# Optimization experiments

Measured on AMD Instinct MI355X. Metric: run time of the kernel, lower is better.

The kernel has to match this reference:

```python
import jax, jax.numpy as jnp
import numpy as np

N_NODES = 50000
N_EDGES = 800000
N_GRAPHS = 1024
H = 128          # hidden_dim
L = 5            # n_conv_layers
NODE_IN = 4
EDGE_IN = 41
N_TARGETS = 3
EPS = 1e-5


def _ln(x, g, b):
    m = jnp.mean(x, axis=-1, keepdims=True)
    v = jnp.var(x, axis=-1, keepdims=True)
    return (x - m) / jnp.sqrt(v + EPS) * g + b


def setup_inputs() -> dict:
    key = jax.random.key(0)
    ks = jax.random.split(key, 24)
    w = lambda k, shp: (jax.random.normal(k, shp, dtype=jnp.float32) * 0.05)
    inp = {
        "atom_fea": jax.random.normal(ks[0], (N_NODES, NODE_IN), dtype=jnp.float32),
        "nbr_fea": jax.random.normal(ks[1], (N_EDGES, EDGE_IN), dtype=jnp.float32),
        "nbr_idx": jax.random.randint(ks[2], (N_EDGES, 2), 0, N_NODES, dtype=jnp.int32),
        "batch_mapping": jnp.sort(jax.random.randint(ks[3], (N_NODES,), 0, N_GRAPHS, dtype=jnp.int32)),
        # node embedding: Linear(4->H) + LayerNorm + SiLU
        "emb_w": w(ks[4], (NODE_IN, H)), "emb_b": jnp.zeros((H,), jnp.float32),
        "emb_ln_g": jnp.ones((H,), jnp.float32), "emb_ln_b": jnp.zeros((H,), jnp.float32),
        # edge embedding: Linear(41->H) + SiLU
        "edge_w": w(ks[5], (EDGE_IN, H)), "edge_b": jnp.zeros((H,), jnp.float32),
        # conv layers: Linear(2H->2H), SiLU, Linear(2H->H), SiLU; stacked over L
        "conv_w1": w(ks[6], (L, 2 * H, 2 * H)), "conv_b1": jnp.zeros((L, 2 * H), jnp.float32),
        "conv_w2": w(ks[7], (L, 2 * H, H)), "conv_b2": jnp.zeros((L, H), jnp.float32),
        "ln_g": jnp.ones((L, H), jnp.float32), "ln_b": jnp.zeros((L, H), jnp.float32),
        # output head
        "out_w1": w(ks[8], (H, H)), "out_b1": jnp.zeros((H,), jnp.float32),
        "out_w2": w(ks[9], (H, H // 2)), "out_b2": jnp.zeros((H // 2,), jnp.float32),
        "out_w3": w(ks[10], (H // 2, N_TARGETS)), "out_b3": jnp.zeros((N_TARGETS,), jnp.float32),
    }
    return inp


def reference(atom_fea, nbr_fea, nbr_idx, batch_mapping,
              emb_w, emb_b, emb_ln_g, emb_ln_b, edge_w, edge_b,
              conv_w1, conv_b1, conv_w2, conv_b2, ln_g, ln_b,
              out_w1, out_b1, out_w2, out_b2, out_w3, out_b3):
    silu = jax.nn.silu
    # embeddings (dropout is eval-mode identity)
    x = silu(_ln(atom_fea @ emb_w + emb_b, emb_ln_g, emb_ln_b))      # [N, H]
    e = silu(nbr_fea @ edge_w + edge_b)                               # [E, H]
    src, dst = nbr_idx[:, 0], nbr_idx[:, 1]
    n = x.shape[0]
    # per-node incoming edge counts (same every layer)
    cnt = jax.ops.segment_sum(jnp.ones_like(dst, dtype=x.dtype), dst, num_segments=n)
    cnt = jnp.clip(cnt, 1.0)[:, None]
    for i in range(L):
        m = jnp.concatenate([x[src], e], axis=1)                      # [E, 2H] gather
        m = silu(m @ conv_w1[i] + conv_b1[i])                         # [E, 2H]
        m = silu(m @ conv_w2[i] + conv_b2[i])                         # [E, H]
        aggr = jax.ops.segment_sum(m, dst, num_segments=n) / cnt      # scatter-mean
        x = _ln(x + aggr, ln_g[i], ln_b[i])                           # residual + LN
    # graph-level mean pooling
    gcnt = jax.ops.segment_sum(jnp.ones((n,), x.dtype), batch_mapping, num_segments=N_GRAPHS)
    gcnt = jnp.clip(gcnt, 1.0)[:, None]
    crystal = jax.ops.segment_sum(x, batch_mapping, num_segments=N_GRAPHS) / gcnt  # [G, H]
    h = silu(crystal @ out_w1 + out_b1)
    h = silu(h @ out_w2 + out_b2)
    return h @ out_w3 + out_b3                                        # [G, n_targets]
```

## Files before the change

### kernel.cpp

```cpp
#include <hip/hip_runtime.h>
#include <hip/hip_bf16.h>
#include <math.h>

#define N_NODES 50000
#define N_EDGES 800000
#define N_GRAPHS 1024
#define HD 128
#define NLAYERS 5
#define EDGE_IN 41
#define NT 3
#define LN_EPS 1e-5f

typedef unsigned int uint;
typedef unsigned short ushort;
typedef __attribute__((ext_vector_type(8))) short short8;
typedef __attribute__((ext_vector_type(4))) float f32x4;
typedef __attribute__((ext_vector_type(4))) ushort us4;

__device__ __forceinline__ float silu_f(float v) {
    return v * __builtin_amdgcn_rcpf(1.0f + __expf(-v));
}

__device__ __forceinline__ ushort f2bf(float f) {
    uint u = __float_as_uint(f);
    u = u + 0x7FFFu + ((u >> 16) & 1u);
    return (ushort)(u >> 16);
}

__device__ __forceinline__ short8 ld16(const ushort* p) {
    union { int4 i; short8 s; } u;
    u.i = *(const int4*)p;
    return u.s;
}

__device__ __forceinline__ f32x4 mfma16(short8 a, short8 b, f32x4 c) {
    return __builtin_amdgcn_mfma_f32_16x16x32_bf16(a, b, c, 0, 0, 0);
}

__device__ __forceinline__ void compiler_fence() {
    __asm__ volatile("" ::: "memory");
}

__device__ __forceinline__ void cp16(const ushort* g, ushort* l) {
    __builtin_amdgcn_global_load_lds(
        (const __attribute__((address_space(1))) unsigned int*)g,
        (__attribute__((address_space(3))) unsigned int*)l, 16, 0, 0);
}

__device__ __forceinline__ void stage4k(ushort* lds, const ushort* g, int w, int L) {
#pragma unroll
    for (int i = 0; i < 2; ++i) {
        int f = w * 1024 + i * 512;
        cp16(g + f + L * 8, lds + f);
    }
}

__global__ void k_zero(float* __restrict__ p, int n) {
    int i = blockIdx.x * 256 + threadIdx.x;
    if (i < n) p[i] = 0.0f;
}

__global__ void k_hist(const int* __restrict__ nbr_idx, int* __restrict__ cnt_i) {
    int i = blockIdx.x * 256 + threadIdx.x;
    if (i < N_EDGES) atomicAdd(&cnt_i[nbr_idx[2 * i + 1]], 1);
}

__global__ __launch_bounds__(1024) void k_scan(
    const int* __restrict__ cnt_i, int* __restrict__ cur, float* __restrict__ cntf)
{
    __shared__ int warpsum[16];
    __shared__ int srun;
    int tid = threadIdx.x;
    int lane = tid & 63, wv = tid >> 6;
    if (tid == 0) srun = 0;
    __syncthreads();
    for (int base = 0; base < N_NODES; base += 1024) {
        int i = base + tid;
        int c = (i < N_NODES) ? cnt_i[i] : 0;
        int s = c;
        for (int off = 1; off < 64; off <<= 1) {
            int t = __shfl_up(s, off);
            if (lane >= off) s += t;
        }
        if (lane == 63) warpsum[wv] = s;
        __syncthreads();
        int woff = 0;
        for (int k = 0; k < wv; ++k) woff += warpsum[k];
        int run = srun;
        if (i < N_NODES) {
            cur[i]  = run + woff + s - c;
            cntf[i] = (float)c;
        }
        __syncthreads();
        if (tid == 1023) srun = run + woff + s;
    }
}

__global__ void k_scatter(const int* __restrict__ nbr_idx, int* __restrict__ cur,
                          int* __restrict__ ssrc, int* __restrict__ sdst,
                          int* __restrict__ posof)
{
    int e = blockIdx.x * 256 + threadIdx.x;
    if (e < N_EDGES) {
        int s = nbr_idx[2 * e];
        int d = nbr_idx[2 * e + 1];
        int p = atomicAdd(&cur[d], 1);
        ssrc[p] = s;
        sdst[p] = d;
        posof[e] = p;
    }
}

__global__ void k_swz_w1(const float* __restrict__ w1, ushort* __restrict__ w1s) {
    int i = blockIdx.x * 256 + threadIdx.x;
    int l = i >> 16;
    int r = i & 65535;
    int j = r & 7, L = (r >> 3) & 63, s = (r >> 9) & 7, c = (r >> 12) & 15;
    int k = 32 * s + ((L >> 4) & 3) * 8 + j;
    int n = 16 * c + (L & 15);
    w1s[i] = f2bf(w1[(size_t)l * 65536 + k * 256 + n]);
}
__global__ void k_swz_w2(const float* __restrict__ w2, ushort* __restrict__ w2s) {
    int i = blockIdx.x * 256 + threadIdx.x;
    int l = i >> 15;
    int r = i & 32767;
    int j = r & 7, L = (r >> 3) & 63, t = (r >> 9) & 7, s2 = (r >> 12) & 7;
    int k = 32 * s2 + ((L >> 4) & 3) * 8 + j;
    int n = 16 * t + (L & 15);
    w2s[i] = f2bf(w2[(size_t)l * 32768 + k * 128 + n]);
}

__global__ __launch_bounds__(128) void k_node_embed(
    const float* __restrict__ atom, const float* __restrict__ w,
    const float* __restrict__ b, const float* __restrict__ g,
    const float* __restrict__ bet, float* __restrict__ x, ushort* __restrict__ x_bf)
{
    int node = blockIdx.x;
    int h = threadIdx.x;
    float4 a = *(const float4*)(atom + (size_t)node * 4);
    float acc = b[h] + a.x * w[h] + a.y * w[HD + h] + a.z * w[2 * HD + h] + a.w * w[3 * HD + h];
    __shared__ float s1[2], s2[2];
    float sum = acc, sq = acc * acc;
    for (int off = 32; off > 0; off >>= 1) { sum += __shfl_down(sum, off); sq += __shfl_down(sq, off); }
    int wid = h >> 6, lane = h & 63;
    if (lane == 0) { s1[wid] = sum; s2[wid] = sq; }
    __syncthreads();
    float m = (s1[0] + s1[1]) * (1.0f / 128.0f);
    float v = (s2[0] + s2[1]) * (1.0f / 128.0f) - m * m;
    float y = (acc - m) * rsqrtf(v + LN_EPS) * g[h] + bet[h];
    y = silu_f(y);
    x[(size_t)node * HD + h] = y;
    x_bf[(size_t)node * HD + h] = f2bf(y);
}

#define ETILE 32
__global__ __launch_bounds__(128) void k_edge_embed(
    const float* __restrict__ fea, const float* __restrict__ w,
    const float* __restrict__ b, const int* __restrict__ posof,
    ushort* __restrict__ e_bf)
{
    __shared__ float sf[ETILE][EDGE_IN + 1];
    int e0 = blockIdx.x * ETILE;
    int tid = threadIdx.x;
    for (int i = tid; i < ETILE * EDGE_IN; i += 128) {
        int m = i / EDGE_IN, k = i % EDGE_IN;
        sf[m][k] = fea[(size_t)(e0 + m) * EDGE_IN + k];
    }
    __syncthreads();
    float bb = b[tid];
    float acc[ETILE];
#pragma unroll
    for (int m = 0; m < ETILE; m++) acc[m] = bb;
    for (int k = 0; k < EDGE_IN; k++) {
        float wk = w[k * HD + tid];
#pragma unroll
        for (int m = 0; m < ETILE; m++) acc[m] += sf[m][k] * wk;
    }
#pragma unroll
    for (int m = 0; m < ETILE; m++) {
        int p = posof[e0 + m];
        e_bf[(size_t)p * HD + tid] = f2bf(silu_f(acc[m]));
    }
}

__global__ void k_gcount(const int* __restrict__ bm, float* __restrict__ gcnt) {
    int i = blockIdx.x * 256 + threadIdx.x;
    if (i < N_NODES) atomicAdd(&gcnt[bm[i]], 1.0f);
}

#define M1CP 40
#define RSTR 18
__global__ __launch_bounds__(256, 3) void k_conv_mfma(
    const ushort* __restrict__ x_bf, const ushort* __restrict__ e_bf,
    const int* __restrict__ ssrc, const int* __restrict__ sdst,
    const ushort* __restrict__ w1s, const float* __restrict__ cb1,
    const ushort* __restrict__ w2s, const float* __restrict__ cb2,
    float* __restrict__ aggr)
{
    __shared__ __align__(16) ushort sW1[2][4096];
    __shared__ __align__(16) ushort sW2[4096];
    __shared__ __align__(16) ushort sM1[4][32 * M1CP];
    __shared__ int sDst[128];

    int tid = threadIdx.x;
    int w = tid >> 6;
    int L = tid & 63;
    int m = L & 15;
    int quad = L >> 4;
    int eb = blockIdx.x * 128;
    int ew = eb + w * 32;

    if (tid < 128) sDst[tid] = sdst[eb + tid];

    short8 af[2][8];
#pragma unroll
    for (int t = 0; t < 2; ++t) {
        int src = ssrc[ew + t * 16 + m];
        const ushort* xr = x_bf + (size_t)src * HD + quad * 8;
        const ushort* er = e_bf + (size_t)(ew + t * 16 + m) * HD + quad * 8;
#pragma unroll
        for (int s = 0; s < 4; ++s) af[t][s] = ld16(xr + 32 * s);
#pragma unroll
        for (int s = 0; s < 4; ++s) af[t][4 + s] = ld16(er + 32 * s);
    }

    f32x4 acc2[2][8];
#pragma unroll
    for (int t = 0; t < 2; ++t)
#pragma unroll
        for (int tt = 0; tt < 8; ++tt)
#pragma unroll
            for (int r = 0; r < 4; ++r) acc2[t][tt][r] = 0.0f;

    ushort* sm = sM1[w];

    stage4k(sW1[0], w1s, w, L);
    stage4k(sW2, w2s, w, L);

    for (int p = 0; p < 16; ++p) {
        __syncthreads();
        if (p < 15) stage4k(sW1[(p + 1) & 1], w1s + (p + 1) * 4096, w, L);
        if (!(p & 1) && p >= 2)
            stage4k(sW2, w2s + (p >> 1) * 4096, w, L);

        f32x4 p0a, p0b, p1a, p1b;
#pragma unroll
        for (int r = 0; r < 4; ++r) { p0a[r] = 0.0f; p0b[r] = 0.0f; p1a[r] = 0.0f; p1b[r] = 0.0f; }
        const ushort* wb = sW1[p & 1] + L * 8;
        __builtin_amdgcn_s_setprio(1);
#pragma unroll
        for (int s = 0; s < 4; ++s) {
            short8 wv = ld16(wb + s * 512);
            p0a = mfma16(af[0][s], wv, p0a);
            p1a = mfma16(af[1][s], wv, p1a);
        }
#pragma unroll
        for (int s = 4; s < 8; ++s) {
            short8 wv = ld16(wb + s * 512);
            p0b = mfma16(af[0][s], wv, p0b);
            p1b = mfma16(af[1][s], wv, p1b);
        }
        __builtin_amdgcn_s_setprio(0);
        f32x4 p0 = p0a + p0b;
        f32x4 p1 = p1a + p1b;

        float bv = cb1[p * 16 + m];
        int hb = (p & 1) * 16;
#pragma unroll
        for (int r = 0; r < 4; ++r) {
            sm[(quad * 4 + r) * M1CP + hb + m]        = f2bf(silu_f(p0[r] + bv));
            sm[(16 + quad * 4 + r) * M1CP + hb + m]   = f2bf(silu_f(p1[r] + bv));
        }

        if (p & 1) {
            compiler_fence();
            short8 a20 = ld16(sm + m * M1CP + quad * 8);
            short8 a21 = ld16(sm + (16 + m) * M1CP + quad * 8);
            const ushort* w2p = sW2 + L * 8;
            __builtin_amdgcn_s_setprio(1);
#pragma unroll
            for (int tt = 0; tt < 8; ++tt) {
                short8 bf = ld16(w2p + tt * 512);
                acc2[0][tt] = mfma16(a20, bf, acc2[0][tt]);
                acc2[1][tt] = mfma16(a21, bf, acc2[1][tt]);
            }
            __builtin_amdgcn_s_setprio(0);
            compiler_fence();
        }
    }

    float* sRed = (float*)sW1;
    int tcol = tid & 15;
    int row0 = (tid >> 4) * 8;
#pragma unroll
    for (int tt = 0; tt < 8; ++tt) {
        __syncthreads();
        float bv = cb2[tt * 16 + m];
#pragma unroll
        for (int t = 0; t < 2; ++t)
#pragma unroll
            for (int r = 0; r < 4; ++r)
                sRed[(w * 32 + t * 16 + quad * 4 + r) * RSTR + m] =
                    silu_f(acc2[t][tt][r] + bv);
        __syncthreads();
        float s = sRed[row0 * RSTR + tcol];
        int cd = sDst[row0];
        for (int i = 1; i < 8; ++i) {
            int rr = row0 + i;
            int d2 = sDst[rr];
            float v = sRed[rr * RSTR + tcol];
            if (d2 == cd) {
                s += v;
            } else {
                atomicAdd(aggr + (size_t)cd * HD + tt * 16 + tcol, s);
                cd = d2;
                s = v;
            }
        }
        atomicAdd(aggr + (size_t)cd * HD + tt * 16 + tcol, s);
    }
}

__global__ __launch_bounds__(256) void k_post(
    float* __restrict__ aggr, const float* __restrict__ cnt,
    const float* __restrict__ g, const float* __restrict__ bet,
    float* __restrict__ x, ushort* __restrict__ x_bf)
{
    int t = threadIdx.x;
    int node = blockIdx.x * 8 + (t >> 5);
    int c = (t & 31) * 4;
    size_t base = (size_t)node * HD + c;
    float inv = __builtin_amdgcn_rcpf(fmaxf(cnt[node], 1.0f));
    f32x4 av = *(f32x4*)(aggr + base);
    f32x4 z; z[0] = 0.0f; z[1] = 0.0f; z[2] = 0.0f; z[3] = 0.0f;
    *(f32x4*)(aggr + base) = z;
    f32x4 xv = *(const f32x4*)(x + base);
    f32x4 acc;
#pragma unroll
    for (int j = 0; j < 4; ++j) acc[j] = xv[j] + av[j] * inv;
    float sum = acc[0] + acc[1] + acc[2] + acc[3];
    float sq  = acc[0]*acc[0] + acc[1]*acc[1] + acc[2]*acc[2] + acc[3]*acc[3];
    for (int off = 16; off > 0; off >>= 1) {
        sum += __shfl_down(sum, off, 32);
        sq  += __shfl_down(sq,  off, 32);
    }
    float msum = __shfl(sum, 0, 32);
    float msq  = __shfl(sq,  0, 32);
    float mean = msum * (1.0f / 128.0f);
    float var  = msq * (1.0f / 128.0f) - mean * mean;
    float rstd = rsqrtf(var + LN_EPS);
    f32x4 gv = *(const f32x4*)(g + c);
    f32x4 bv = *(const f32x4*)(bet + c);
    f32x4 y;
    us4 ybf;
#pragma unroll
    for (int j = 0; j < 4; ++j) {
        y[j] = (acc[j] - mean) * rstd * gv[j] + bv[j];
        ybf[j] = f2bf(y[j]);
    }
    *(f32x4*)(x + base) = y;
    *(us4*)(x_bf + base) = ybf;
}

__global__ __launch_bounds__(128) void k_gaggr(
    const float* __restrict__ x, const int* __restrict__ bm,
    float* __restrict__ crystal)
{
    int node = blockIdx.x;
    int h = threadIdx.x;
    atomicAdd(&crystal[(size_t)bm[node] * HD + h], x[(size_t)node * HD + h]);
}

__global__ __launch_bounds__(128) void k_readout(
    const float* __restrict__ crystal, const float* __restrict__ gcnt,
    const float* __restrict__ w1, const float* __restrict__ b1,
    const float* __restrict__ w2, const float* __restrict__ b2,
    const float* __restrict__ w3, const float* __restrict__ b3,
    float* __restrict__ out)
{
    int gph = blockIdx.x;
    int t = threadIdx.x;
    __shared__ float sc[HD], sh1[HD], sh2[64];
    float inv = __builtin_amdgcn_rcpf(fmaxf(gcnt[gph], 1.0f));
    sc[t] = crystal[(size_t)gph * HD + t] * inv;
    __syncthreads();
    float acc = b1[t];
    for (int k = 0; k < HD; k++) acc += sc[k] * w1[k * HD + t];
    sh1[t] = silu_f(acc);
    __syncthreads();
    if (t < 64) {
        float a2 = b2[t];
        for (int k = 0; k < HD; k++) a2 += sh1[k] * w2[k * 64 + t];
        sh2[t] = silu_f(a2);
    }
    __syncthreads();
    if (t < NT) {
        float a3 = b3[t];
        for (int k = 0; k < 64; k++) a3 += sh2[k] * w3[k * NT + t];
        out[(size_t)gph * NT + t] = a3;
    }
}

extern "C" void kernel_launch(void* const* d_in, const int* in_sizes, int n_in,
                              void* d_out, int out_size, void* d_ws, size_t ws_size,
                              hipStream_t stream)
{
    const float* atom_fea = (const float*)d_in[0];
    const float* nbr_fea  = (const float*)d_in[1];
    const int*   nbr_idx  = (const int*)d_in[2];
    const int*   bm       = (const int*)d_in[3];
    const float* emb_w    = (const float*)d_in[4];
    const float* emb_b    = (const float*)d_in[5];
    const float* emb_ln_g = (const float*)d_in[6];
    const float* emb_ln_b = (const float*)d_in[7];
    const float* edge_w   = (const float*)d_in[8];
    const float* edge_b   = (const float*)d_in[9];
    const float* conv_w1  = (const float*)d_in[10];
    const float* conv_b1  = (const float*)d_in[11];
    const float* conv_w2  = (const float*)d_in[12];
    const float* conv_b2  = (const float*)d_in[13];
    const float* ln_g     = (const float*)d_in[14];
    const float* ln_b     = (const float*)d_in[15];
    const float* out_w1   = (const float*)d_in[16];
    const float* out_b1   = (const float*)d_in[17];
    const float* out_w2   = (const float*)d_in[18];
    const float* out_b2   = (const float*)d_in[19];
    const float* out_w3   = (const float*)d_in[20];
    const float* out_b3   = (const float*)d_in[21];
    float* out = (float*)d_out;

    char* base = (char*)d_ws;
    size_t off = 0;
    auto alloc = [&](size_t bytes) -> char* {
        char* p = base + off;
        off = (off + bytes + 255) & ~(size_t)255;
        return p;
    };
    float*  xbuf    = (float*) alloc((size_t)N_NODES * HD * 4);
    float*  aggr    = (float*) alloc((size_t)N_NODES * HD * 4);
    float*  cnt     = (float*) alloc((size_t)N_NODES * 4);
    float*  crystal = (float*) alloc((size_t)N_GRAPHS * HD * 4);
    float*  gcnt    = (float*) alloc((size_t)N_GRAPHS * 4);
    ushort* x_bf    = (ushort*)alloc((size_t)N_NODES * HD * 2);
    ushort* e_bf    = (ushort*)alloc((size_t)N_EDGES * HD * 2);
    ushort* w1s     = (ushort*)alloc((size_t)NLAYERS * 65536 * 2);
    ushort* w2s     = (ushort*)alloc((size_t)NLAYERS * 32768 * 2);
    int*    cnt_i   = (int*)   alloc((size_t)N_NODES * 4);
    int*    cur     = (int*)   alloc((size_t)N_NODES * 4);
    int*    ssrc    = (int*)   alloc((size_t)N_EDGES * 4);
    int*    sdst    = (int*)   alloc((size_t)N_EDGES * 4);
    int*    posof   = (int*)   alloc((size_t)N_EDGES * 4);

    k_swz_w1<<<(NLAYERS * 65536) / 256, 256, 0, stream>>>(conv_w1, w1s);
    k_swz_w2<<<(NLAYERS * 32768) / 256, 256, 0, stream>>>(conv_w2, w2s);

    k_zero<<<(N_NODES * HD) / 256, 256, 0, stream>>>(aggr, N_NODES * HD);
    int zn = N_NODES + N_GRAPHS * HD + N_GRAPHS + 128;
    k_zero<<<(zn + 255) / 256, 256, 0, stream>>>(cnt, zn);
    k_zero<<<(N_NODES + 255) / 256, 256, 0, stream>>>((float*)cnt_i, N_NODES);

    k_hist<<<N_EDGES / 256, 256, 0, stream>>>(nbr_idx, cnt_i);
    k_scan<<<1, 1024, 0, stream>>>(cnt_i, cur, cnt);
    k_scatter<<<N_EDGES / 256, 256, 0, stream>>>(nbr_idx, cur, ssrc, sdst, posof);

    k_node_embed<<<N_NODES, 128, 0, stream>>>(atom_fea, emb_w, emb_b, emb_ln_g, emb_ln_b, xbuf, x_bf);
    k_edge_embed<<<N_EDGES / ETILE, 128, 0, stream>>>(nbr_fea, edge_w, edge_b, posof, e_bf);
    k_gcount<<<(N_NODES + 255) / 256, 256, 0, stream>>>(bm, gcnt);

    for (int l = 0; l < NLAYERS; ++l) {
        k_conv_mfma<<<N_EDGES / 128, 256, 0, stream>>>(
            x_bf, e_bf, ssrc, sdst,
            w1s + (size_t)l * 65536, conv_b1 + (size_t)l * 256,
            w2s + (size_t)l * 32768, conv_b2 + (size_t)l * 128,
            aggr);
        k_post<<<N_NODES / 8, 256, 0, stream>>>(aggr, cnt, ln_g + (size_t)l * HD, ln_b + (size_t)l * HD, xbuf, x_bf);
    }

    k_gaggr<<<N_NODES, 128, 0, stream>>>(xbuf, bm, crystal);
    k_readout<<<N_GRAPHS, 128, 0, stream>>>(crystal, gcnt, out_w1, out_b1, out_w2, out_b2, out_w3, out_b3, out);
}
```

Measured before the change: 2.251 ms.

## Read conv weights from global directly, drop LDS staging and fuse pooling into post

The conv kernel no longer stages W1/W2 tiles into LDS with async global-to-LDS copies and per-step barriers. Each lane now loads its weight fragments straight from global memory (L2/L1 cached), which removes the barriers from the main loop and shrinks LDS use so more blocks can be resident. The reduction epilogue alternates between two LDS buffers, which drops one barrier per column tile. Separately, the graph mean-pooling atomics move into the last k_post launch, removing the k_gaggr kernel. The risk is extra global load latency and traffic, since every wave now re-reads the weights.

```diff
diff --git a/kernel.cpp b/kernel.cpp
--- a/kernel.cpp
+++ b/kernel.cpp
@@ -39,20 +39,6 @@
 
 __device__ __forceinline__ void compiler_fence() {
     __asm__ volatile("" ::: "memory");
-}
-
-__device__ __forceinline__ void cp16(const ushort* g, ushort* l) {
-    __builtin_amdgcn_global_load_lds(
-        (const __attribute__((address_space(1))) unsigned int*)g,
-        (__attribute__((address_space(3))) unsigned int*)l, 16, 0, 0);
-}
-
-__device__ __forceinline__ void stage4k(ushort* lds, const ushort* g, int w, int L) {
-#pragma unroll
-    for (int i = 0; i < 2; ++i) {
-        int f = w * 1024 + i * 512;
-        cp16(g + f + L * 8, lds + f);
-    }
 }
 
 __global__ void k_zero(float* __restrict__ p, int n) {
@@ -197,9 +183,8 @@
     const ushort* __restrict__ w2s, const float* __restrict__ cb2,
     float* __restrict__ aggr)
 {
-    __shared__ __align__(16) ushort sW1[2][4096];
-    __shared__ __align__(16) ushort sW2[4096];
     __shared__ __align__(16) ushort sM1[4][32 * M1CP];
+    __shared__ __align__(16) float sRed[128 * RSTR];
     __shared__ int sDst[128];
 
     int tid = threadIdx.x;
@@ -233,34 +218,30 @@
             for (int r = 0; r < 4; ++r) acc2[t][tt][r] = 0.0f;
 
     ushort* sm = sM1[w];
-
-    stage4k(sW1[0], w1s, w, L);
-    stage4k(sW2, w2s, w, L);
+    const ushort* gw1 = w1s + L * 8;
+    const ushort* gw2 = w2s + L * 8;
 
     for (int p = 0; p < 16; ++p) {
-        __syncthreads();
-        if (p < 15) stage4k(sW1[(p + 1) & 1], w1s + (p + 1) * 4096, w, L);
-        if (!(p & 1) && p >= 2)
-            stage4k(sW2, w2s + (p >> 1) * 4096, w, L);
-
+        const ushort* wp = gw1 + p * 4096;
+        short8 wv0 = ld16(wp);
+        short8 wv1 = ld16(wp + 512);
+        short8 wv2 = ld16(wp + 1024);
+        short8 wv3 = ld16(wp + 1536);
+        short8 wv4 = ld16(wp + 2048);
+        short8 wv5 = ld16(wp + 2560);
+        short8 wv6 = ld16(wp + 3072);
+        short8 wv7 = ld16(wp + 3584);
         f32x4 p0a, p0b, p1a, p1b;
 #pragma unroll
         for (int r = 0; r < 4; ++r) { p0a[r] = 0.0f; p0b[r] = 0.0f; p1a[r] = 0.0f; p1b[r] = 0.0f; }
-        const ushort* wb = sW1[p & 1] + L * 8;
-        __builtin_amdgcn_s_setprio(1);
-#pragma unroll
-        for (int s = 0; s < 4; ++s) {
-            short8 wv = ld16(wb + s * 512);
-            p0a = mfma16(af[0][s], wv, p0a);
-            p1a = mfma16(af[1][s], wv, p1a);
-        }
-#pragma unroll
-        for (int s = 4; s < 8; ++s) {
-            short8 wv = ld16(wb + s * 512);
-            p0b = mfma16(af[0][s], wv, p0b);
-            p1b = mfma16(af[1][s], wv, p1b);
-        }
-        __builtin_amdgcn_s_setprio(0);
+        p0a = mfma16(af[0][0], wv0, p0a);  p1a = mfma16(af[1][0], wv0, p1a);
+        p0a = mfma16(af[0][1], wv1, p0a);  p1a = mfma16(af[1][1], wv1, p1a);
+        p0a = mfma16(af[0][2], wv2, p0a);  p1a = mfma16(af[1][2], wv2, p1a);
+        p0a = mfma16(af[0][3], wv3, p0a);  p1a = mfma16(af[1][3], wv3, p1a);
+        p0b = mfma16(af[0][4], wv4, p0b);  p1b = mfma16(af[1][4], wv4, p1b);
+        p0b = mfma16(af[0][5], wv5, p0b);  p1b = mfma16(af[1][5], wv5, p1b);
+        p0b = mfma16(af[0][6], wv6, p0b);  p1b = mfma16(af[1][6], wv6, p1b);
+        p0b = mfma16(af[0][7], wv7, p0b);  p1b = mfma16(af[1][7], wv7, p1b);
         f32x4 p0 = p0a + p0b;
         f32x4 p1 = p1a + p1b;
 
@@ -276,39 +257,37 @@
             compiler_fence();
             short8 a20 = ld16(sm + m * M1CP + quad * 8);
             short8 a21 = ld16(sm + (16 + m) * M1CP + quad * 8);
-            const ushort* w2p = sW2 + L * 8;
-            __builtin_amdgcn_s_setprio(1);
+            const ushort* w2p = gw2 + (p >> 1) * 4096;
 #pragma unroll
             for (int tt = 0; tt < 8; ++tt) {
                 short8 bf = ld16(w2p + tt * 512);
                 acc2[0][tt] = mfma16(a20, bf, acc2[0][tt]);
                 acc2[1][tt] = mfma16(a21, bf, acc2[1][tt]);
             }
-            __builtin_amdgcn_s_setprio(0);
             compiler_fence();
         }
     }
 
-    float* sRed = (float*)sW1;
     int tcol = tid & 15;
     int row0 = (tid >> 4) * 8;
+    __syncthreads();
 #pragma unroll
     for (int tt = 0; tt < 8; ++tt) {
-        __syncthreads();
+        float* rb = (tt & 1) ? (float*)&sM1[0][0] : sRed;
         float bv = cb2[tt * 16 + m];
 #pragma unroll
         for (int t = 0; t < 2; ++t)
 #pragma unroll
             for (int r = 0; r < 4; ++r)
-                sRed[(w * 32 + t * 16 + quad * 4 + r) * RSTR + m] =
+                rb[(w * 32 + t * 16 + quad * 4 + r) * RSTR + m] =
                     silu_f(acc2[t][tt][r] + bv);
         __syncthreads();
-        float s = sRed[row0 * RSTR + tcol];
+        float s = rb[row0 * RSTR + tcol];
         int cd = sDst[row0];
         for (int i = 1; i < 8; ++i) {
             int rr = row0 + i;
             int d2 = sDst[rr];
-            float v = sRed[rr * RSTR + tcol];
+            float v = rb[rr * RSTR + tcol];
             if (d2 == cd) {
                 s += v;
             } else {
@@ -324,7 +303,8 @@
 __global__ __launch_bounds__(256) void k_post(
     float* __restrict__ aggr, const float* __restrict__ cnt,
     const float* __restrict__ g, const float* __restrict__ bet,
-    float* __restrict__ x, ushort* __restrict__ x_bf)
+    float* __restrict__ x, ushort* __restrict__ x_bf,
+    const int* __restrict__ bm, float* __restrict__ crystal, int last)
 {
     int t = threadIdx.x;
     int node = blockIdx.x * 8 + (t >> 5);
@@ -360,15 +340,12 @@
     }
     *(f32x4*)(x + base) = y;
     *(us4*)(x_bf + base) = ybf;
-}
-
-__global__ __launch_bounds__(128) void k_gaggr(
-    const float* __restrict__ x, const int* __restrict__ bm,
-    float* __restrict__ crystal)
-{
-    int node = blockIdx.x;
-    int h = threadIdx.x;
-    atomicAdd(&crystal[(size_t)bm[node] * HD + h], x[(size_t)node * HD + h]);
+    if (last) {
+        int gph = bm[node];
+        float* cp = crystal + (size_t)gph * HD + c;
+#pragma unroll
+        for (int j = 0; j < 4; ++j) atomicAdd(cp + j, y[j]);
+    }
 }
 
 __global__ __launch_bounds__(128) void k_readout(
@@ -473,9 +450,9 @@
             w1s + (size_t)l * 65536, conv_b1 + (size_t)l * 256,
             w2s + (size_t)l * 32768, conv_b2 + (size_t)l * 128,
             aggr);
-        k_post<<<N_NODES / 8, 256, 0, stream>>>(aggr, cnt, ln_g + (size_t)l * HD, ln_b + (size_t)l * HD, xbuf, x_bf);
-    }
-
-    k_gaggr<<<N_NODES, 128, 0, stream>>>(xbuf, bm, crystal);
+        k_post<<<N_NODES / 8, 256, 0, stream>>>(aggr, cnt, ln_g + (size_t)l * HD, ln_b + (size_t)l * HD,
+                                                xbuf, x_bf, bm, crystal, (l == NLAYERS - 1) ? 1 : 0);
+    }
+
     k_readout<<<N_GRAPHS, 128, 0, stream>>>(crystal, gcnt, out_w1, out_b1, out_w2, out_b2, out_w3, out_b3, out);
 }
```

Result: slower. 3.036 ms (+34.9%).

## Feed first-MLP output to second GEMM in registers and fuse graph pooling

Applied to the files above, without the earlier changes.

The first conv GEMM now computes the transposed product (weights as the A operand), so each lane's output lands directly in the register layout the 16x16x16 bf16 MFMA expects for the second GEMM. This removes the per-warp LDS round trip for the hidden activations and its fence. W2 is re-swizzled into 16-row k-slices and double-buffered alongside W1 each step. Graph mean-pool accumulation moves into the last post-layer kernel, dropping a separate launch and the re-read of x. The trade-off is twice as many smaller-K MFMA instructions for the second GEMM, and the removal of the setprio hints.

```diff
diff --git a/kernel.cpp b/kernel.cpp
--- a/kernel.cpp
+++ b/kernel.cpp
@@ -14,6 +14,7 @@
 typedef unsigned int uint;
 typedef unsigned short ushort;
 typedef __attribute__((ext_vector_type(8))) short short8;
+typedef __attribute__((ext_vector_type(4))) short s4bf;
 typedef __attribute__((ext_vector_type(4))) float f32x4;
 typedef __attribute__((ext_vector_type(4))) ushort us4;
 
@@ -33,12 +34,25 @@
     return u.s;
 }
 
+__device__ __forceinline__ s4bf ld8(const ushort* p) {
+    union { uint2 i; s4bf s; } u;
+    u.i = *(const uint2*)p;
+    return u.s;
+}
+
+__device__ __forceinline__ s4bf pack4(float a, float b, float c, float d) {
+    union { uint u[2]; s4bf s; } x;
+    x.u[0] = (uint)f2bf(a) | ((uint)f2bf(b) << 16);
+    x.u[1] = (uint)f2bf(c) | ((uint)f2bf(d) << 16);
+    return x.s;
+}
+
 __device__ __forceinline__ f32x4 mfma16(short8 a, short8 b, f32x4 c) {
     return __builtin_amdgcn_mfma_f32_16x16x32_bf16(a, b, c, 0, 0, 0);
 }
 
-__device__ __forceinline__ void compiler_fence() {
-    __asm__ volatile("" ::: "memory");
+__device__ __forceinline__ f32x4 mfma_k16(s4bf a, s4bf b, f32x4 c) {
+    return __builtin_amdgcn_mfma_f32_16x16x16bf16_1k(a, b, c, 0, 0, 0);
 }
 
 __device__ __forceinline__ void cp16(const ushort* g, ushort* l) {
@@ -53,6 +67,10 @@
         int f = w * 1024 + i * 512;
         cp16(g + f + L * 8, lds + f);
     }
+}
+__device__ __forceinline__ void stage2k(ushort* lds, const ushort* g, int w, int L) {
+    int f = w * 512;
+    cp16(g + f + L * 8, lds + f);
 }
 
 __global__ void k_zero(float* __restrict__ p, int n) {
@@ -124,9 +142,9 @@
     int i = blockIdx.x * 256 + threadIdx.x;
     int l = i >> 15;
     int r = i & 32767;
-    int j = r & 7, L = (r >> 3) & 63, t = (r >> 9) & 7, s2 = (r >> 12) & 7;
-    int k = 32 * s2 + ((L >> 4) & 3) * 8 + j;
-    int n = 16 * t + (L & 15);
+    int j = r & 3, L = (r >> 2) & 63, t2 = (r >> 8) & 7, p = (r >> 11) & 15;
+    int k = p * 16 + ((L >> 4) & 3) * 4 + j;
+    int n = t2 * 16 + (L & 15);
     w2s[i] = f2bf(w2[(size_t)l * 32768 + k * 128 + n]);
 }
 
@@ -188,7 +206,6 @@
     if (i < N_NODES) atomicAdd(&gcnt[bm[i]], 1.0f);
 }
 
-#define M1CP 40
 #define RSTR 18
 __global__ __launch_bounds__(256, 3) void k_conv_mfma(
     const ushort* __restrict__ x_bf, const ushort* __restrict__ e_bf,
@@ -198,8 +215,8 @@
     float* __restrict__ aggr)
 {
     __shared__ __align__(16) ushort sW1[2][4096];
-    __shared__ __align__(16) ushort sW2[4096];
-    __shared__ __align__(16) ushort sM1[4][32 * M1CP];
+    __shared__ __align__(16) ushort sW2[2][2048];
+    __shared__ __align__(16) float sRed[128 * RSTR];
     __shared__ int sDst[128];
 
     int tid = threadIdx.x;
@@ -232,64 +249,50 @@
 #pragma unroll
             for (int r = 0; r < 4; ++r) acc2[t][tt][r] = 0.0f;
 
-    ushort* sm = sM1[w];
-
     stage4k(sW1[0], w1s, w, L);
-    stage4k(sW2, w2s, w, L);
+    stage2k(sW2[0], w2s, w, L);
 
     for (int p = 0; p < 16; ++p) {
         __syncthreads();
-        if (p < 15) stage4k(sW1[(p + 1) & 1], w1s + (p + 1) * 4096, w, L);
-        if (!(p & 1) && p >= 2)
-            stage4k(sW2, w2s + (p >> 1) * 4096, w, L);
-
+        if (p < 15) {
+            stage4k(sW1[(p + 1) & 1], w1s + (p + 1) * 4096, w, L);
+            stage2k(sW2[(p + 1) & 1], w2s + (p + 1) * 2048, w, L);
+        }
+
+        const ushort* wb = sW1[p & 1] + L * 8;
         f32x4 p0a, p0b, p1a, p1b;
 #pragma unroll
         for (int r = 0; r < 4; ++r) { p0a[r] = 0.0f; p0b[r] = 0.0f; p1a[r] = 0.0f; p1b[r] = 0.0f; }
-        const ushort* wb = sW1[p & 1] + L * 8;
-        __builtin_amdgcn_s_setprio(1);
 #pragma unroll
         for (int s = 0; s < 4; ++s) {
             short8 wv = ld16(wb + s * 512);
-            p0a = mfma16(af[0][s], wv, p0a);
-            p1a = mfma16(af[1][s], wv, p1a);
+            p0a = mfma16(wv, af[0][s], p0a);
+            p1a = mfma16(wv, af[1][s], p1a);
         }
 #pragma unroll
         for (int s = 4; s < 8; ++s) {
             short8 wv = ld16(wb + s * 512);
-            p0b = mfma16(af[0][s], wv, p0b);
-            p1b = mfma16(af[1][s], wv, p1b);
-        }
-        __builtin_amdgcn_s_setprio(0);
+            p0b = mfma16(wv, af[0][s], p0b);
+            p1b = mfma16(wv, af[1][s], p1b);
+        }
         f32x4 p0 = p0a + p0b;
         f32x4 p1 = p1a + p1b;
 
-        float bv = cb1[p * 16 + m];
-        int hb = (p & 1) * 16;
-#pragma unroll
-        for (int r = 0; r < 4; ++r) {
-            sm[(quad * 4 + r) * M1CP + hb + m]        = f2bf(silu_f(p0[r] + bv));
-            sm[(16 + quad * 4 + r) * M1CP + hb + m]   = f2bf(silu_f(p1[r] + bv));
-        }
-
-        if (p & 1) {
-            compiler_fence();
-            short8 a20 = ld16(sm + m * M1CP + quad * 8);
-            short8 a21 = ld16(sm + (16 + m) * M1CP + quad * 8);
-            const ushort* w2p = sW2 + L * 8;
-            __builtin_amdgcn_s_setprio(1);
-#pragma unroll
-            for (int tt = 0; tt < 8; ++tt) {
-                short8 bf = ld16(w2p + tt * 512);
-                acc2[0][tt] = mfma16(a20, bf, acc2[0][tt]);
-                acc2[1][tt] = mfma16(a21, bf, acc2[1][tt]);
-            }
-            __builtin_amdgcn_s_setprio(0);
-            compiler_fence();
-        }
-    }
-
-    float* sRed = (float*)sW1;
+        float4 bv4 = *(const float4*)(cb1 + p * 16 + quad * 4);
+        s4bf pa0 = pack4(silu_f(p0[0] + bv4.x), silu_f(p0[1] + bv4.y),
+                         silu_f(p0[2] + bv4.z), silu_f(p0[3] + bv4.w));
+        s4bf pa1 = pack4(silu_f(p1[0] + bv4.x), silu_f(p1[1] + bv4.y),
+                         silu_f(p1[2] + bv4.z), silu_f(p1[3] + bv4.w));
+
+        const ushort* w2p = sW2[p & 1] + L * 4;
+#pragma unroll
+        for (int tt = 0; tt < 8; ++tt) {
+            s4bf bf = ld8(w2p + tt * 256);
+            acc2[0][tt] = mfma_k16(pa0, bf, acc2[0][tt]);
+            acc2[1][tt] = mfma_k16(pa1, bf, acc2[1][tt]);
+        }
+    }
+
     int tcol = tid & 15;
     int row0 = (tid >> 4) * 8;
 #pragma unroll
@@ -324,7 +327,8 @@
 __global__ __launch_bounds__(256) void k_post(
     float* __restrict__ aggr, const float* __restrict__ cnt,
     const float* __restrict__ g, const float* __restrict__ bet,
-    float* __restrict__ x, ushort* __restrict__ x_bf)
+    float* __restrict__ x, ushort* __restrict__ x_bf,
+    const int* __restrict__ bm, float* __restrict__ crystal, int last)
 {
     int t = threadIdx.x;
     int node = blockIdx.x * 8 + (t >> 5);
@@ -360,15 +364,12 @@
     }
     *(f32x4*)(x + base) = y;
     *(us4*)(x_bf + base) = ybf;
-}
-
-__global__ __launch_bounds__(128) void k_gaggr(
-    const float* __restrict__ x, const int* __restrict__ bm,
-    float* __restrict__ crystal)
-{
-    int node = blockIdx.x;
-    int h = threadIdx.x;
-    atomicAdd(&crystal[(size_t)bm[node] * HD + h], x[(size_t)node * HD + h]);
+    if (last) {
+        int gph = bm[node];
+        float* cp = crystal + (size_t)gph * HD + c;
+#pragma unroll
+        for (int j = 0; j < 4; ++j) atomicAdd(cp + j, y[j]);
+    }
 }
 
 __global__ __launch_bounds__(128) void k_readout(
@@ -473,9 +474,9 @@
             w1s + (size_t)l * 65536, conv_b1 + (size_t)l * 256,
             w2s + (size_t)l * 32768, conv_b2 + (size_t)l * 128,
             aggr);
-        k_post<<<N_NODES / 8, 256, 0, stream>>>(aggr, cnt, ln_g + (size_t)l * HD, ln_b + (size_t)l * HD, xbuf, x_bf);
-    }
-
-    k_gaggr<<<N_NODES, 128, 0, stream>>>(xbuf, bm, crystal);
+        k_post<<<N_NODES / 8, 256, 0, stream>>>(aggr, cnt, ln_g + (size_t)l * HD, ln_b + (size_t)l * HD,
+                                                xbuf, x_bf, bm, crystal, (l == NLAYERS - 1) ? 1 : 0);
+    }
+
     k_readout<<<N_GRAPHS, 128, 0, stream>>>(crystal, gcnt, out_w1, out_b1, out_w2, out_b2, out_w3, out_b3, out);
 }
```

After: 2.425 ms. +7.7%, slower.
